# Kernel optimization log

Measured on AMD Instinct MI355X. Metric: run time of the kernel, lower is better.

Reference implementation:

```python
import jax, jax.numpy as jnp
import numpy as np

N_NODES = 100000
IN_CH = 128
HID = 128
OUT_CH = 40
K = 3
N_EDGES = 3200000


def setup_inputs() -> dict:
    key = jax.random.key(0)
    ks = jax.random.split(key, 10)
    x = jax.random.normal(ks[0], (N_NODES, IN_CH), dtype=jnp.float32)
    edge_index = jax.random.randint(ks[1], (2, N_EDGES), 0, N_NODES, dtype=jnp.int64)
    s1 = 1.0 / np.sqrt(IN_CH)
    lin1_w = jax.random.uniform(ks[2], (IN_CH, HID), minval=-s1, maxval=s1, dtype=jnp.float32)
    lin1_b = jax.random.uniform(ks[3], (HID,), minval=-s1, maxval=s1, dtype=jnp.float32)
    s2 = 1.0 / np.sqrt(HID)
    gcn_w = jax.random.uniform(ks[4], (K, HID, HID), minval=-s2, maxval=s2, dtype=jnp.float32)
    gcn_b = jnp.zeros((K, HID), dtype=jnp.float32)
    lin2_w = jax.random.uniform(ks[5], (HID, OUT_CH), minval=-s2, maxval=s2, dtype=jnp.float32)
    lin2_b = jax.random.uniform(ks[6], (OUT_CH,), minval=-s2, maxval=s2, dtype=jnp.float32)
    return {"x": x, "edge_index": edge_index, "lin1_w": lin1_w, "lin1_b": lin1_b,
            "gcn_w": gcn_w, "gcn_b": gcn_b, "lin2_w": lin2_w, "lin2_b": lin2_b}


def _gcn_conv(h, w, b, src, dst, norm, n):
    # PyG GCNConv: transform, then symmetric-normalized aggregation (self-loops
    # already included in src/dst/norm), then bias.
    h = h @ w  # [N, H]
    msg = h[src] * norm[:, None]  # [E+N, H] gathered edge messages
    out = jax.ops.segment_sum(msg, dst, num_segments=n)
    return out + b


def reference(x, edge_index, lin1_w, lin1_b, gcn_w, gcn_b, lin2_w, lin2_b):
    n = x.shape[0]
    src, dst = edge_index[0], edge_index[1]
    # add self-loops (GCNConv default add_self_loops=True)
    loop = jnp.arange(n, dtype=src.dtype)
    src = jnp.concatenate([src, loop])
    dst = jnp.concatenate([dst, loop])
    # symmetric normalization D^{-1/2} (A+I) D^{-1/2}
    deg = jax.ops.segment_sum(jnp.ones(src.shape[0], dtype=x.dtype), dst, num_segments=n)
    dinv = jnp.where(deg > 0, jax.lax.rsqrt(deg), 0.0)
    norm = dinv[src] * dinv[dst]  # [E+N]

    h = jax.nn.relu(x @ lin1_w + lin1_b)  # dropout: eval mode (identity)
    for k in range(K):
        h = jax.nn.relu(_gcn_conv(h, gcn_w[k], gcn_b[k], src, dst, norm, n))
    logits = h @ lin2_w + lin2_b
    return jax.nn.log_softmax(logits, axis=1)
```

## Files before the change

kernel.cpp:

```cpp
#include <hip/hip_runtime.h>
#include <math.h>

#define NN 100000
#define NP 100032
#define HIDC 128
#define OUTC 40
#define NBUCK ((NN + 511) >> 9)
#define PT_TILE 4096
#define BCAP 18368

typedef __attribute__((ext_vector_type(2))) float floatx2;
typedef __attribute__((ext_vector_type(4))) float floatx4;
typedef __attribute__((ext_vector_type(8))) short short8;

__device__ __forceinline__ unsigned pack_bf16x2(float a, float b) {
  unsigned ua = __float_as_uint(a), ub = __float_as_uint(b);
  ua = ua + 0x7fff + ((ua >> 16) & 1);
  ub = ub + 0x7fff + ((ub >> 16) & 1);
  return (ua >> 16) | (ub & 0xffff0000u);
}
__device__ __forceinline__ unsigned short bf16r(float x) {
  unsigned u = __float_as_uint(x);
  u = u + 0x7fff + ((u >> 16) & 1);
  return (unsigned short)(u >> 16);
}


__global__ __launch_bounds__(256) void partition_kernel(
    const int* __restrict__ src, const int* __restrict__ dst,
    int* __restrict__ bcur, unsigned* __restrict__ pairs, int E) {
  __shared__ int hist[256];
  __shared__ int base[256];
  __shared__ int lcur[256];
  int t = threadIdx.x;
  hist[t] = 0; lcur[t] = 0;
  __syncthreads();
  int e0 = blockIdx.x * PT_TILE;
  int ec = E - e0; if (ec > PT_TILE) ec = PT_TILE;
  for (int i = t; i < ec; i += 256)
    atomicAdd(&hist[dst[e0 + i] >> 9], 1);
  __syncthreads();
  if (hist[t] > 0) base[t] = atomicAdd(&bcur[t], hist[t]);
  __syncthreads();
  for (int i = t; i < ec; i += 256) {
    int d = dst[e0 + i], s = src[e0 + i];
    int b = d >> 9;
    int pos = atomicAdd(&lcur[b], 1);
    pairs[base[b] + pos] = ((unsigned)(d & 511) << 17) | (unsigned)s;
  }
}

__global__ __launch_bounds__(1024) void bucket_fill_kernel(
    const unsigned* __restrict__ pairs, const int* __restrict__ bcur,
    float* __restrict__ dinv, int* __restrict__ csr,
    int* __restrict__ sbeg, int* __restrict__ send,
    float* __restrict__ sdinv, int* __restrict__ sdn, int N) {
  int b = blockIdx.x;
  int d0 = b << 9;
  int nd = N - d0; if (nd > 512) nd = 512;
  __shared__ int hist[512];
  __shared__ int cur[512];
  __shared__ int sums[512];
  int t = threadIdx.x;
  if (t < 512) hist[t] = 0;
  __syncthreads();
  int rbeg = b * BCAP, rend = bcur[b];
  for (int i = rbeg + t; i < rend; i += 1024)
    atomicAdd(&hist[pairs[i] >> 17], 1);
  __syncthreads();
  int h = 0;
  if (t < 512) { h = hist[t]; sums[t] = h; }
  __syncthreads();
  for (int off = 1; off < 512; off <<= 1) {
    int u = (t < 512 && t >= off) ? sums[t - off] : 0;
    __syncthreads();
    if (t < 512) sums[t] += u;
    __syncthreads();
  }
  int base = 0; float di = 0.f;
  if (t < 512) {
    base = rbeg + sums[t] - h;
    di = rsqrtf((float)(h + 1));
    if (t < nd) { dinv[d0 + t] = di; cur[t] = base; }
  }
  __syncthreads();

  if (t < 128) hist[t] = 0;
  __syncthreads();
  int c = h < 127 ? h : 127;
  if (t < nd) atomicAdd(&hist[c], 1);
  __syncthreads();
  int dv = (t < 128) ? hist[t] : 0;
  if (t < 128) sums[t] = dv;
  __syncthreads();
  for (int off = 1; off < 128; off <<= 1) {
    int u = (t < 128 && t >= off) ? sums[t - off] : 0;
    __syncthreads();
    if (t < 128) sums[t] += u;
    __syncthreads();
  }
  if (t < 128) hist[128 + t] = sums[t] - dv;
  __syncthreads();
  if (t < nd) {
    int pos = d0 + atomicAdd(&hist[128 + c], 1);
    sbeg[pos] = base; send[pos] = base + h; sdinv[pos] = di; sdn[pos] = d0 + t;
  }
  __syncthreads();

  for (int i = rbeg + t; i < rend; i += 1024) {
    unsigned pk = pairs[i];
    int q = atomicAdd(&cur[pk >> 17], 1);
    csr[q] = pk & 0x1FFFF;
  }
}


__global__ __launch_bounds__(256) void prep_misc_kernel(
    const float* __restrict__ lin1_w, const float* __restrict__ gcn_w,
    const float* __restrict__ lin2_w, int* __restrict__ bcur,
    unsigned short* __restrict__ Wt, unsigned short* __restrict__ W2t) {
  int b = blockIdx.x;
  int t = threadIdx.x;
  if (b == 0) {
    if (t < NBUCK) bcur[t] = t * BCAP;
  } else if (b <= 32) {
    int m = (b - 1) >> 3;
    int chunk = (b - 1) & 7;
    const float* src = (m == 0) ? lin1_w : (gcn_w + (size_t)(m - 1) * 16384);
    unsigned short* dstp = Wt + (size_t)m * 16384;
    int i0 = chunk * 2048;
    for (int i = i0 + t; i < i0 + 2048; i += 256) {
      int n = i >> 7, k = i & 127;
      dstp[(size_t)n * 128 + k] = bf16r(src[(size_t)k * 128 + n]);
    }
  } else {
    int chunk = b - 33;
    int i0 = chunk * 3072;
    for (int i = i0 + t; i < i0 + 3072; i += 256) {
      int n = i >> 7, k = i & 127;
      W2t[i] = (n < OUTC) ? bf16r(lin2_w[(size_t)k * OUTC + n]) : (unsigned short)0;
    }
  }
}


template <int MODE>
__global__ __launch_bounds__(256) void gemm_mfma_kernel(
    const void* __restrict__ Av, const unsigned short* __restrict__ Wt,
    const float* __restrict__ bias, const float* __restrict__ dinv,
    void* __restrict__ Y, int M) {
  int t = threadIdx.x;
  int w = t >> 6;
  int l = t & 63;
  int quad = l >> 4;
  int m16 = l & 15;
  int row0 = blockIdx.x * 64;
  int colbase = w * 32;

  floatx4 acc[4][2];
#pragma unroll
  for (int rt = 0; rt < 4; rt++)
#pragma unroll
    for (int ct = 0; ct < 2; ct++) acc[rt][ct] = (floatx4)0.f;

#pragma unroll
  for (int kc = 0; kc < 4; kc++) {
    int kof = kc * 32 + quad * 8;
    short8 a0 = *(const short8*)(Wt + (size_t)(colbase + m16) * 128 + kof);
    short8 a1 = *(const short8*)(Wt + (size_t)(colbase + 16 + m16) * 128 + kof);
#pragma unroll
    for (int rt = 0; rt < 4; rt++) {
      short8 bfr;
      if (MODE == 2) {
        const float* Af = (const float*)Av + (size_t)(row0 + rt * 16 + m16) * 128 + kof;
        float4 f0 = *(const float4*)Af;
        float4 f1 = *(const float4*)(Af + 4);
        unsigned u0 = pack_bf16x2(f0.x, f0.y);
        unsigned u1 = pack_bf16x2(f0.z, f0.w);
        unsigned u2 = pack_bf16x2(f1.x, f1.y);
        unsigned u3 = pack_bf16x2(f1.z, f1.w);
        bfr[0] = (short)(u0 & 0xFFFF); bfr[1] = (short)(u0 >> 16);
        bfr[2] = (short)(u1 & 0xFFFF); bfr[3] = (short)(u1 >> 16);
        bfr[4] = (short)(u2 & 0xFFFF); bfr[5] = (short)(u2 >> 16);
        bfr[6] = (short)(u3 & 0xFFFF); bfr[7] = (short)(u3 >> 16);
      } else {
        bfr = *(const short8*)((const unsigned short*)Av +
                               (size_t)(row0 + rt * 16 + m16) * 128 + kof);
      }
      acc[rt][0] = __builtin_amdgcn_mfma_f32_16x16x32_bf16(a0, bfr, acc[rt][0], 0, 0, 0);
      acc[rt][1] = __builtin_amdgcn_mfma_f32_16x16x32_bf16(a1, bfr, acc[rt][1], 0, 0, 0);
    }
  }

  if (MODE != 1) {
    unsigned short* Y16 = (unsigned short*)Y;
    float4 bv0 = *(const float4*)(bias + colbase + quad * 4);
    float4 bv1 = *(const float4*)(bias + colbase + 16 + quad * 4);
#pragma unroll
    for (int rt = 0; rt < 4; rt++) {
      int row = row0 + rt * 16 + m16;
      if (row < M) {
        uint2 s0, s1;
        s0.x = pack_bf16x2(fmaxf(acc[rt][0][0] + bv0.x, 0.f),
                           fmaxf(acc[rt][0][1] + bv0.y, 0.f));
        s0.y = pack_bf16x2(fmaxf(acc[rt][0][2] + bv0.z, 0.f),
                           fmaxf(acc[rt][0][3] + bv0.w, 0.f));
        s1.x = pack_bf16x2(fmaxf(acc[rt][1][0] + bv1.x, 0.f),
                           fmaxf(acc[rt][1][1] + bv1.y, 0.f));
        s1.y = pack_bf16x2(fmaxf(acc[rt][1][2] + bv1.z, 0.f),
                           fmaxf(acc[rt][1][3] + bv1.w, 0.f));
        *(uint2*)(Y16 + (size_t)row * 128 + colbase + quad * 4) = s0;
        *(uint2*)(Y16 + (size_t)row * 128 + colbase + 16 + quad * 4) = s1;
      }
    }
  } else {
    unsigned* Y8 = (unsigned*)Y;
#pragma unroll
    for (int rt = 0; rt < 4; rt++) {
      int row = row0 + rt * 16 + m16;
      if (row < M) {
        float dd = dinv[row];
        unsigned u0 = 0, u1 = 0;
        u0 = __builtin_amdgcn_cvt_pk_fp8_f32(acc[rt][0][0] * dd, acc[rt][0][1] * dd, (int)u0, false);
        u0 = __builtin_amdgcn_cvt_pk_fp8_f32(acc[rt][0][2] * dd, acc[rt][0][3] * dd, (int)u0, true);
        u1 = __builtin_amdgcn_cvt_pk_fp8_f32(acc[rt][1][0] * dd, acc[rt][1][1] * dd, (int)u1, false);
        u1 = __builtin_amdgcn_cvt_pk_fp8_f32(acc[rt][1][2] * dd, acc[rt][1][3] * dd, (int)u1, true);
        Y8[(size_t)row * 32 + (colbase >> 2) + quad] = u0;
        Y8[(size_t)row * 32 + ((colbase + 16) >> 2) + quad] = u1;
      }
    }
  }
}


#define ACC8(u)                                                       \
  acc[0] += __builtin_amdgcn_cvt_pk_f32_fp8((int)(u).x, false);       \
  acc[1] += __builtin_amdgcn_cvt_pk_f32_fp8((int)(u).x, true);        \
  acc[2] += __builtin_amdgcn_cvt_pk_f32_fp8((int)(u).y, false);       \
  acc[3] += __builtin_amdgcn_cvt_pk_f32_fp8((int)(u).y, true);        \
  acc[4] += __builtin_amdgcn_cvt_pk_f32_fp8((int)(u).z, false);       \
  acc[5] += __builtin_amdgcn_cvt_pk_f32_fp8((int)(u).z, true);        \
  acc[6] += __builtin_amdgcn_cvt_pk_f32_fp8((int)(u).w, false);       \
  acc[7] += __builtin_amdgcn_cvt_pk_f32_fp8((int)(u).w, true);

__global__ __launch_bounds__(128) void aggregate_fp8_kernel(
    const uint4* __restrict__ Ht8, const int* __restrict__ csr,
    const int* __restrict__ sbeg, const int* __restrict__ send,
    const float* __restrict__ sdinv, const int* __restrict__ sdn,
    const float* __restrict__ bias, uint4* __restrict__ Out, int N) {
  int wid = (blockIdx.x * blockDim.x + threadIdx.x) >> 6;
  int lane = threadIdx.x & 63;
  int g = lane >> 3;
  int c8 = lane & 7;
  int idx = wid * 8 + g;
  if (idx >= N) return;
  int beg = sbeg[idx], end = send[idx];
  int d = sdn[idx];

  floatx2 acc[8];
  {
    uint4 us = Ht8[(size_t)d * 8 + c8];
    acc[0] = __builtin_amdgcn_cvt_pk_f32_fp8((int)us.x, false);
    acc[1] = __builtin_amdgcn_cvt_pk_f32_fp8((int)us.x, true);
    acc[2] = __builtin_amdgcn_cvt_pk_f32_fp8((int)us.y, false);
    acc[3] = __builtin_amdgcn_cvt_pk_f32_fp8((int)us.y, true);
    acc[4] = __builtin_amdgcn_cvt_pk_f32_fp8((int)us.z, false);
    acc[5] = __builtin_amdgcn_cvt_pk_f32_fp8((int)us.z, true);
    acc[6] = __builtin_amdgcn_cvt_pk_f32_fp8((int)us.w, false);
    acc[7] = __builtin_amdgcn_cvt_pk_f32_fp8((int)us.w, true);
  }
  int i = beg;
  for (; i + 3 < end; i += 4) {
    int s0 = csr[i], s1 = csr[i + 1], s2 = csr[i + 2], s3 = csr[i + 3];
    uint4 u0 = Ht8[(size_t)s0 * 8 + c8];
    uint4 u1 = Ht8[(size_t)s1 * 8 + c8];
    uint4 u2 = Ht8[(size_t)s2 * 8 + c8];
    uint4 u3 = Ht8[(size_t)s3 * 8 + c8];
    ACC8(u0) ACC8(u1) ACC8(u2) ACC8(u3)
  }
  if (i + 1 < end) {
    int s0 = csr[i], s1 = csr[i + 1];
    uint4 u0 = Ht8[(size_t)s0 * 8 + c8];
    uint4 u1 = Ht8[(size_t)s1 * 8 + c8];
    ACC8(u0) ACC8(u1)
    i += 2;
  }
  if (i < end) {
    uint4 u0 = Ht8[(size_t)csr[i] * 8 + c8];
    ACC8(u0)
  }

  float dd = sdinv[idx];
  const float4* b4 = (const float4*)bias;
  float4 bv0 = b4[4 * c8 + 0];
  float4 bv1 = b4[4 * c8 + 1];
  float4 bv2 = b4[4 * c8 + 2];
  float4 bv3 = b4[4 * c8 + 3];
  uint4 o0, o1;
  o0.x = pack_bf16x2(fmaxf(fmaf(dd, acc[0][0], bv0.x), 0.f),
                     fmaxf(fmaf(dd, acc[0][1], bv0.y), 0.f));
  o0.y = pack_bf16x2(fmaxf(fmaf(dd, acc[1][0], bv0.z), 0.f),
                     fmaxf(fmaf(dd, acc[1][1], bv0.w), 0.f));
  o0.z = pack_bf16x2(fmaxf(fmaf(dd, acc[2][0], bv1.x), 0.f),
                     fmaxf(fmaf(dd, acc[2][1], bv1.y), 0.f));
  o0.w = pack_bf16x2(fmaxf(fmaf(dd, acc[3][0], bv1.z), 0.f),
                     fmaxf(fmaf(dd, acc[3][1], bv1.w), 0.f));
  o1.x = pack_bf16x2(fmaxf(fmaf(dd, acc[4][0], bv2.x), 0.f),
                     fmaxf(fmaf(dd, acc[4][1], bv2.y), 0.f));
  o1.y = pack_bf16x2(fmaxf(fmaf(dd, acc[5][0], bv2.z), 0.f),
                     fmaxf(fmaf(dd, acc[5][1], bv2.w), 0.f));
  o1.z = pack_bf16x2(fmaxf(fmaf(dd, acc[6][0], bv3.x), 0.f),
                     fmaxf(fmaf(dd, acc[6][1], bv3.y), 0.f));
  o1.w = pack_bf16x2(fmaxf(fmaf(dd, acc[7][0], bv3.z), 0.f),
                     fmaxf(fmaf(dd, acc[7][1], bv3.w), 0.f));
  Out[(size_t)d * 16 + 2 * c8] = o0;
  Out[(size_t)d * 16 + 2 * c8 + 1] = o1;
}


__global__ __launch_bounds__(256) void head_mfma_kernel(
    const unsigned short* __restrict__ A, const unsigned short* __restrict__ W2t,
    const float* __restrict__ b2, float* __restrict__ Out, int N) {
  __shared__ float lg[64][48];
  __shared__ float bs[48];
  int t = threadIdx.x;
  int w = t >> 6, l = t & 63, quad = l >> 4, m16 = l & 15;
  if (t < 48) bs[t] = (t < OUTC) ? b2[t] : 0.f;
  int row0 = blockIdx.x * 64;

  floatx4 acc[3];
  acc[0] = (floatx4)0.f; acc[1] = (floatx4)0.f; acc[2] = (floatx4)0.f;
  const unsigned short* Aw = A + (size_t)(row0 + w * 16) * 128;
#pragma unroll
  for (int kc = 0; kc < 4; kc++) {
    int kof = kc * 32 + quad * 8;
    short8 a = *(const short8*)(Aw + (size_t)m16 * 128 + kof);
#pragma unroll
    for (int ct = 0; ct < 3; ct++) {
      short8 b = *(const short8*)(W2t + (size_t)(ct * 16 + m16) * 128 + kof);
      acc[ct] = __builtin_amdgcn_mfma_f32_16x16x32_bf16(a, b, acc[ct], 0, 0, 0);
    }
  }
#pragma unroll
  for (int ct = 0; ct < 3; ct++)
#pragma unroll
    for (int j = 0; j < 4; j++)
      lg[w * 16 + quad * 4 + j][ct * 16 + m16] = acc[ct][j];
  __syncthreads();

  int r = t >> 2, sub = t & 3;
  int row = row0 + r;
  float vals[10];
  float mx = -3.4e38f;
#pragma unroll
  for (int j = 0; j < 10; j++) {
    float v = lg[r][sub * 10 + j] + bs[sub * 10 + j];
    vals[j] = v;
    mx = fmaxf(mx, v);
  }
  mx = fmaxf(mx, __shfl_xor(mx, 1, 64));
  mx = fmaxf(mx, __shfl_xor(mx, 2, 64));
  float se = 0.f;
#pragma unroll
  for (int j = 0; j < 10; j++) se += expf(vals[j] - mx);
  se += __shfl_xor(se, 1, 64);
  se += __shfl_xor(se, 2, 64);
  if (row < N) {
    float ls = logf(se);
#pragma unroll
    for (int j = 0; j < 10; j++)
      Out[(size_t)row * OUTC + sub * 10 + j] = vals[j] - mx - ls;
  }
}


extern "C" void kernel_launch(void* const* d_in, const int* in_sizes, int n_in,
                              void* d_out, int out_size, void* d_ws, size_t ws_size,
                              hipStream_t stream) {
  const float* x      = (const float*)d_in[0];
  const int*   edge   = (const int*)d_in[1];
  const float* lin1_w = (const float*)d_in[2];
  const float* lin1_b = (const float*)d_in[3];
  const float* gcn_w  = (const float*)d_in[4];
  const float* gcn_b  = (const float*)d_in[5];
  const float* lin2_w = (const float*)d_in[6];
  const float* lin2_b = (const float*)d_in[7];
  float* out = (float*)d_out;

  const int N = NN;
  const int E = in_sizes[1] / 2;
  const int* src = edge;
  const int* dst = edge + E;

  char* p = (char*)d_ws;
  auto alloc = [&](size_t bytes) { char* q = p; p += (bytes + 255) & ~(size_t)255; return q; };
  unsigned*       hA16    = (unsigned*)alloc((size_t)NP * 128 * 2);
  unsigned*       hB8     = (unsigned*)alloc((size_t)NP * 32 * 4);
  unsigned*       pairs   = (unsigned*)alloc((size_t)NBUCK * BCAP * 4);
  int*            csr     = (int*)alloc((size_t)NBUCK * BCAP * 4);
  float*          dinv    = (float*)alloc((size_t)NP * 4);
  int*            sbeg    = (int*)alloc((size_t)N * 4);
  int*            send    = (int*)alloc((size_t)N * 4);
  float*          sdinv   = (float*)alloc((size_t)N * 4);
  int*            sdn     = (int*)alloc((size_t)N * 4);
  unsigned short* Wt      = (unsigned short*)alloc((size_t)4 * 16384 * 2);
  unsigned short* W2t     = (unsigned short*)alloc((size_t)48 * 128 * 2);
  int*            bcur    = (int*)alloc(256 * 4);

  prep_misc_kernel<<<35, 256, 0, stream>>>(lin1_w, gcn_w, lin2_w, bcur, Wt, W2t);
  partition_kernel<<<(E + PT_TILE - 1) / PT_TILE, 256, 0, stream>>>(src, dst, bcur, pairs, E);
  bucket_fill_kernel<<<NBUCK, 1024, 0, stream>>>(pairs, bcur, dinv, csr,
                                                 sbeg, send, sdinv, sdn, N);

  int gb = NP / 64;
  gemm_mfma_kernel<2><<<gb, 256, 0, stream>>>((const void*)x, Wt,
                                              lin1_b, nullptr, (void*)hA16, N);
  int ablocks = (N / 8 + 1) / 2;
  for (int k = 0; k < 3; k++) {
    gemm_mfma_kernel<1><<<gb, 256, 0, stream>>>((const void*)hA16,
                                                Wt + (size_t)(k + 1) * 16384,
                                                nullptr, dinv, (void*)hB8, N);
    aggregate_fp8_kernel<<<ablocks, 128, 0, stream>>>(
        (const uint4*)hB8, csr, sbeg, send, sdinv, sdn, gcn_b + (size_t)k * 128,
        (uint4*)hA16, N);
  }
  head_mfma_kernel<<<gb, 256, 0, stream>>>((const unsigned short*)hA16, W2t,
                                           lin2_b, out, N);
}
```

Before: 506.8 us.

## Split CSR scatter into grid-wide kernel, prefetch indices, enlarge aggregate blocks

Result: slower. 577.4 us (+13.9%).

```diff
diff --git a/kernel.cpp b/kernel.cpp
--- a/kernel.cpp
+++ b/kernel.cpp
@@ -6,7 +6,7 @@
 #define HIDC 128
 #define OUTC 40
 #define NBUCK ((NN + 511) >> 9)
-#define PT_TILE 4096
+#define PT_TILE 2048
 #define BCAP 18368
 
 typedef __attribute__((ext_vector_type(2))) float floatx2;
@@ -52,14 +52,13 @@
 
 __global__ __launch_bounds__(1024) void bucket_fill_kernel(
     const unsigned* __restrict__ pairs, const int* __restrict__ bcur,
-    float* __restrict__ dinv, int* __restrict__ csr,
+    float* __restrict__ dinv, int* __restrict__ cur_g,
     int* __restrict__ sbeg, int* __restrict__ send,
     float* __restrict__ sdinv, int* __restrict__ sdn, int N) {
   int b = blockIdx.x;
   int d0 = b << 9;
   int nd = N - d0; if (nd > 512) nd = 512;
   __shared__ int hist[512];
-  __shared__ int cur[512];
   __shared__ int sums[512];
   int t = threadIdx.x;
   if (t < 512) hist[t] = 0;
@@ -81,7 +80,7 @@
   if (t < 512) {
     base = rbeg + sums[t] - h;
     di = rsqrtf((float)(h + 1));
-    if (t < nd) { dinv[d0 + t] = di; cur[t] = base; }
+    if (t < nd) { dinv[d0 + t] = di; cur_g[d0 + t] = base; }
   }
   __syncthreads();
 
@@ -105,13 +104,18 @@
     int pos = d0 + atomicAdd(&hist[128 + c], 1);
     sbeg[pos] = base; send[pos] = base + h; sdinv[pos] = di; sdn[pos] = d0 + t;
   }
-  __syncthreads();
-
-  for (int i = rbeg + t; i < rend; i += 1024) {
-    unsigned pk = pairs[i];
-    int q = atomicAdd(&cur[pk >> 17], 1);
-    csr[q] = pk & 0x1FFFF;
-  }
+}
+
+__global__ __launch_bounds__(256) void csr_scatter_kernel(
+    const unsigned* __restrict__ pairs, const int* __restrict__ bcur,
+    int* __restrict__ cur_g, int* __restrict__ csr) {
+  int b = blockIdx.y;
+  int i = b * BCAP + blockIdx.x * 256 + threadIdx.x;
+  if (i >= bcur[b]) return;
+  unsigned pk = pairs[i];
+  int node = (b << 9) + (int)(pk >> 17);
+  int q = atomicAdd(&cur_g[node], 1);
+  csr[q] = pk & 0x1FFFF;
 }
 
 
@@ -243,7 +247,7 @@
   acc[6] += __builtin_amdgcn_cvt_pk_f32_fp8((int)(u).w, false);       \
   acc[7] += __builtin_amdgcn_cvt_pk_f32_fp8((int)(u).w, true);
 
-__global__ __launch_bounds__(128) void aggregate_fp8_kernel(
+__global__ __launch_bounds__(256) void aggregate_fp8_kernel(
     const uint4* __restrict__ Ht8, const int* __restrict__ csr,
     const int* __restrict__ sbeg, const int* __restrict__ send,
     const float* __restrict__ sdinv, const int* __restrict__ sdn,
@@ -270,22 +274,18 @@
     acc[7] = __builtin_amdgcn_cvt_pk_f32_fp8((int)us.w, true);
   }
   int i = beg;
-  for (; i + 3 < end; i += 4) {
-    int s0 = csr[i], s1 = csr[i + 1], s2 = csr[i + 2], s3 = csr[i + 3];
+  int s0 = 0, s1 = 0, s2 = 0, s3 = 0;
+  if (i + 3 < end) { s0 = csr[i]; s1 = csr[i + 1]; s2 = csr[i + 2]; s3 = csr[i + 3]; }
+  while (i + 3 < end) {
     uint4 u0 = Ht8[(size_t)s0 * 8 + c8];
     uint4 u1 = Ht8[(size_t)s1 * 8 + c8];
     uint4 u2 = Ht8[(size_t)s2 * 8 + c8];
     uint4 u3 = Ht8[(size_t)s3 * 8 + c8];
+    i += 4;
+    if (i + 3 < end) { s0 = csr[i]; s1 = csr[i + 1]; s2 = csr[i + 2]; s3 = csr[i + 3]; }
     ACC8(u0) ACC8(u1) ACC8(u2) ACC8(u3)
   }
-  if (i + 1 < end) {
-    int s0 = csr[i], s1 = csr[i + 1];
-    uint4 u0 = Ht8[(size_t)s0 * 8 + c8];
-    uint4 u1 = Ht8[(size_t)s1 * 8 + c8];
-    ACC8(u0) ACC8(u1)
-    i += 2;
-  }
-  if (i < end) {
+  for (; i < end; ++i) {
     uint4 u0 = Ht8[(size_t)csr[i] * 8 + c8];
     ACC8(u0)
   }
@@ -399,6 +399,7 @@
   unsigned*       pairs   = (unsigned*)alloc((size_t)NBUCK * BCAP * 4);
   int*            csr     = (int*)alloc((size_t)NBUCK * BCAP * 4);
   float*          dinv    = (float*)alloc((size_t)NP * 4);
+  int*            cur_g   = (int*)alloc((size_t)NP * 4);
   int*            sbeg    = (int*)alloc((size_t)N * 4);
   int*            send    = (int*)alloc((size_t)N * 4);
   float*          sdinv   = (float*)alloc((size_t)N * 4);
@@ -409,18 +410,20 @@
 
   prep_misc_kernel<<<35, 256, 0, stream>>>(lin1_w, gcn_w, lin2_w, bcur, Wt, W2t);
   partition_kernel<<<(E + PT_TILE - 1) / PT_TILE, 256, 0, stream>>>(src, dst, bcur, pairs, E);
-  bucket_fill_kernel<<<NBUCK, 1024, 0, stream>>>(pairs, bcur, dinv, csr,
+  bucket_fill_kernel<<<NBUCK, 1024, 0, stream>>>(pairs, bcur, dinv, cur_g,
                                                  sbeg, send, sdinv, sdn, N);
+  dim3 sg((BCAP + 255) / 256, NBUCK);
+  csr_scatter_kernel<<<sg, 256, 0, stream>>>(pairs, bcur, cur_g, csr);
 
   int gb = NP / 64;
   gemm_mfma_kernel<2><<<gb, 256, 0, stream>>>((const void*)x, Wt,
                                               lin1_b, nullptr, (void*)hA16, N);
-  int ablocks = (N / 8 + 1) / 2;
+  int ablocks = (N / 8 + 3) / 4;
   for (int k = 0; k < 3; k++) {
     gemm_mfma_kernel<1><<<gb, 256, 0, stream>>>((const void*)hA16,
                                                 Wt + (size_t)(k + 1) * 16384,
                                                 nullptr, dinv, (void*)hB8, N);
-    aggregate_fp8_kernel<<<ablocks, 128, 0, stream>>>(
+    aggregate_fp8_kernel<<<ablocks, 256, 0, stream>>>(
         (const uint4*)hB8, csr, sbeg, send, sdinv, sdn, gcn_b + (size_t)k * 128,
         (uint4*)hA16, N);
   }
```
